# Kernel tuning notes

Hardware: AMD Instinct MI355X
Metric: run time of the kernel (lower is better)

## Reference

```python
import jax, jax.numpy as jnp
import numpy as np

R, E, NU, NI = 5, 50000, 20000, 20000
NF, DN, DR, DO = 4, 16, 64, 64   # num_factor, node/msg dim (64//NF), review dim (msg_units*NF), out_units
TAU = 0.5


def _l2norm(x):
    n = jnp.maximum(jnp.linalg.norm(x, axis=-1, keepdims=True), 1e-12)
    return x / n


def setup_inputs() -> dict:
    key = jax.random.key(0)
    ks = jax.random.split(key, 18)
    s = 0.1  # keep exp() arguments in a sane range / xavier-ish weight scale
    return {
        "user_h": jax.random.normal(ks[0], (NF, R, NU, DN), jnp.float32),
        "item_h": jax.random.normal(ks[1], (NF, R, NI, DN), jnp.float32),
        "user_hsum": jax.random.normal(ks[2], (R, NU, NF, DN), jnp.float32) * s,
        "item_hsum": jax.random.normal(ks[3], (R, NI, NF, DN), jnp.float32) * s,
        "review_feat": jax.random.normal(ks[4], (R, E, NF, DR), jnp.float32) * s,
        "prototypes": jax.random.normal(ks[5], (NF, DR), jnp.float32) * s,
        "eta": jax.random.normal(ks[6], (R, E), jnp.float32),
        "node_w_fwd": jax.random.normal(ks[7], (R, DN, DN), jnp.float32) * s,
        "review_w_fwd": jax.random.normal(ks[8], (R, DN, DR), jnp.float32) * s,
        "node_w_rev": jax.random.normal(ks[9], (R, DN, DN), jnp.float32) * s,
        "review_w_rev": jax.random.normal(ks[10], (R, DN, DR), jnp.float32) * s,
        "ufc_w": jax.random.normal(ks[11], (DO, DN), jnp.float32) * s,
        "ufc_b": jnp.zeros((DO,), jnp.float32),
        "ifc_w": jax.random.normal(ks[12], (DO, DN), jnp.float32) * s,
        "ifc_b": jnp.zeros((DO,), jnp.float32),
        "edge_src": jax.random.randint(ks[13], (R, E), 0, NU),
        "edge_dst": jax.random.randint(ks[14], (R, E), 0, NI),
        "k": 1,
    }


def reference(user_h, item_h, user_hsum, item_hsum, review_feat, prototypes,
              eta, node_w_fwd, review_w_fwd, node_w_rev, review_w_rev,
              ufc_w, ufc_b, ifc_w, ifc_b, edge_src, edge_dst, k):
    rI = jnp.arange(R)[:, None]                       # [R,1] rating index for gathers
    uh, ih = user_h[k], item_h[k]                     # [R,N,DN]
    # contrastive similarity on factor k (L2-normalized node feats)
    row_f = _l2norm(uh[rI, edge_src])                 # [R,E,DN]
    col_f = _l2norm(ih[rI, edge_dst])
    sim_k = jnp.sum(row_f * col_f, -1) / TAU          # [R,E]
    row_all = user_hsum[rI, edge_src]                 # [R,E,NF,DN]
    col_all = item_hsum[rI, edge_dst]
    sim_all = jnp.sum(row_all * col_all, -1) / TAU    # [R,E,NF]
    exp_sim = jnp.exp(sim_k) / jnp.sum(jnp.exp(sim_all), -1)
    # prototype (anchor) similarity of review features
    rf_k = review_feat[:, :, k, :]                    # [R,E,DR]
    anchor_k = jnp.einsum('red,d->re', rf_k, prototypes[k]) / TAU
    anchor_all = jnp.einsum('refd,fd->ref', review_feat, prototypes) / TAU
    exp_anchor = jnp.exp(anchor_k) / jnp.sum(jnp.exp(anchor_all), -1)
    g = jax.nn.sigmoid(eta)                           # eta[rating][:E]
    # identical for 'rating' and 'rev-rating' etypes (all dots commute under row/col swap)
    blended = g * exp_anchor + (1.0 - g) * exp_sim    # [R,E]
    flat = blended.reshape(-1)
    src_flat = edge_src.reshape(-1)
    dst_flat = edge_dst.reshape(-1)
    # fwd and rev etypes each contribute an identical scatter; (x + x) / 2 == x
    norm_user = jax.ops.segment_sum(flat, src_flat, num_segments=NU)
    norm_item = jax.ops.segment_sum(flat, dst_flat, num_segments=NI)
    n_ij = jnp.sqrt(norm_user[edge_src] * norm_item[edge_dst])  # [R,E]
    w = blended / n_ij                                # edge weight, same for both directions
    int_dist = w.reshape(R * E, 1)                    # concat of rev-etype weights in rating order
    # GCMCGraphConv per etype: (node_w(h_src)[row] + review_w(rf)) * w, scatter-sum to dst
    hu = jnp.einsum('rnd,rod->rno', uh, node_w_fwd)   # Linear: x @ W.T, per rating
    hi = jnp.einsum('rnd,rod->rno', ih, node_w_rev)
    rfw = jnp.einsum('red,rod->reo', rf_k, review_w_fwd)
    rfr = jnp.einsum('red,rod->reo', rf_k, review_w_rev)
    m_fwd = (hu[rI, edge_src] + rfw) * w[..., None]   # [R,E,DN] user->item messages
    m_rev = (hi[rI, edge_dst] + rfr) * w[..., None]   # item->user messages
    item_msg = jax.ops.segment_sum(m_fwd.reshape(-1, DN), dst_flat, num_segments=NI)
    user_msg = jax.ops.segment_sum(m_rev.reshape(-1, DN), src_flat, num_segments=NU)
    ufeat = jax.nn.leaky_relu(user_msg, 0.1) @ ufc_w.T + ufc_b
    ifeat = jax.nn.leaky_relu(item_msg, 0.1) @ ifc_w.T + ifc_b
    return ufeat, ifeat, int_dist
```

## Files before the change

### kernel.cpp

```cpp
#include <hip/hip_runtime.h>
#include <math.h>

constexpr int R  = 5;
constexpr int E  = 50000;
constexpr int NU = 20000;
constexpr int NI = 20000;
constexpr int NF = 4;
constexpr int DN = 16;
constexpr int DR = 64;
constexpr int DO = 64;
constexpr float TAU = 0.5f;
constexpr float INV_TAU = 2.0f;

__global__ __launch_bounds__(256) void pass1_kernel(
    const float* __restrict__ user_h,
    const float* __restrict__ item_h,
    const float* __restrict__ user_hsum,
    const float* __restrict__ item_hsum,
    const float* __restrict__ review_feat,
    const float* __restrict__ prototypes,
    const float* __restrict__ eta,
    const int*   __restrict__ edge_src,
    const int*   __restrict__ edge_dst,
    const int*   __restrict__ kptr,
    float* __restrict__ blended_out,
    float* __restrict__ norm_user,
    float* __restrict__ norm_item)
{
    const int lane = threadIdx.x & 63;
    const int w    = threadIdx.x >> 6;
    const int r    = blockIdx.y;
    const int base = (blockIdx.x * 4 + w) * 4;
    const int k    = *kptr;

    const int e  = lane >> 4;
    const int le = lane & 15;
    const int f  = le >> 2;
    const int j  = le & 3;

    const int ee = base + e;
    const long long re = (long long)r * E + ee;

    const int src = edge_src[re];
    const int dst = edge_dst[re];

    float na = 0.f, nb = 0.f, ab = 0.f;
    if (f == 0) {
        const float4 ua = *(const float4*)(user_h + (((long long)k * R + r) * NU + src) * DN + j * 4);
        const float4 ia = *(const float4*)(item_h + (((long long)k * R + r) * NI + dst) * DN + j * 4);
        na = ua.x*ua.x + ua.y*ua.y + ua.z*ua.z + ua.w*ua.w;
        nb = ia.x*ia.x + ia.y*ia.y + ia.z*ia.z + ia.w*ia.w;
        ab = ua.x*ia.x + ua.y*ia.y + ua.z*ia.z + ua.w*ia.w;
    }
    na += __shfl_xor(na, 1, 64); na += __shfl_xor(na, 2, 64);
    nb += __shfl_xor(nb, 1, 64); nb += __shfl_xor(nb, 2, 64);
    ab += __shfl_xor(ab, 1, 64); ab += __shfl_xor(ab, 2, 64);

    const float4 rs = *(const float4*)(user_hsum + ((long long)r * NU + src) * (NF * DN) + le * 4);
    const float4 cs = *(const float4*)(item_hsum + ((long long)r * NI + dst) * (NF * DN) + le * 4);
    float p = rs.x*cs.x + rs.y*cs.y + rs.z*cs.z + rs.w*cs.w;
    p += __shfl_xor(p, 1, 64); p += __shfl_xor(p, 2, 64);
    float denom_sim = __expf(p * INV_TAU);
    denom_sim += __shfl_xor(denom_sim, 4, 64);
    denom_sim += __shfl_xor(denom_sim, 8, 64);

    const float4* rf4 = (const float4*)review_feat + re * (NF * DR / 4);
    const float4* pr4 = (const float4*)prototypes;
    float q = 0.f;
#pragma unroll
    for (int c = 0; c < 4; ++c) {
        const float4 a = rf4[f * 16 + c * 4 + j];
        const float4 b = pr4[f * 16 + c * 4 + j];
        q += a.x*b.x + a.y*b.y + a.z*b.z + a.w*b.w;
    }
    q += __shfl_xor(q, 1, 64); q += __shfl_xor(q, 2, 64);
    float ea = __expf(q * INV_TAU);
    float denom_anc = ea;
    denom_anc += __shfl_xor(denom_anc, 4, 64);
    denom_anc += __shfl_xor(denom_anc, 8, 64);
    const float ea_k = __shfl(ea, (lane & 48) | (k << 2), 64);

    if (le == 0) {
        const float sim_k = ab / (fmaxf(sqrtf(na), 1e-12f) * fmaxf(sqrtf(nb), 1e-12f)) * INV_TAU;
        const float exp_anchor = ea_k / denom_anc;
        const float exp_sim    = __expf(sim_k) / denom_sim;
        const float g = 1.0f / (1.0f + __expf(-eta[re]));
        const float blended = g * exp_anchor + (1.0f - g) * exp_sim;
        blended_out[re] = blended;
        atomicAdd(&norm_user[src], blended);
        atomicAdd(&norm_item[dst], blended);
    }
}

__global__ __launch_bounds__(256) void nodexf_kernel(
    const float* __restrict__ user_h,
    const float* __restrict__ item_h,
    const float* __restrict__ node_w_fwd,
    const float* __restrict__ node_w_rev,
    const int*   __restrict__ kptr,
    float* __restrict__ hu_t,
    float* __restrict__ hi_t)
{
    const int r    = blockIdx.y;
    const int side = blockIdx.z;
    const int n0   = blockIdx.x * 64;
    const int k    = *kptr;
    const int N    = side ? NI : NU;
    const float* h    = side ? item_h : user_h;
    const float* wsrc = side ? node_w_rev : node_w_fwd;
    float* out        = side ? hi_t : hu_t;

    __shared__ __align__(16) float lds_h[64 * 16];
    __shared__ float lds_w[16 * 17];

    const int t = threadIdx.x;
    {
        const int o = t >> 4, d = t & 15;
        lds_w[o * 17 + d] = wsrc[((long long)r * DN + o) * DN + d];
    }
    {
        const int row = t >> 2, c = t & 3;
        if (n0 + row < N) {
            const float4 v = *(const float4*)(h + (((long long)k * R + r) * N + n0 + row) * DN + c * 4);
            *(float4*)&lds_h[t * 4] = v;
        }
    }
    __syncthreads();

    const int o = t & 15;
#pragma unroll
    for (int p = 0; p < 4; ++p) {
        const int nl = p * 16 + (t >> 4);
        const int n = n0 + nl;
        if (n < N) {
            float acc = 0.f;
#pragma unroll
            for (int d = 0; d < DN; ++d)
                acc += lds_h[nl * 16 + d] * lds_w[o * 17 + d];
            out[((long long)r * N + n) * DN + o] = acc;
        }
    }
}

__global__ __launch_bounds__(256) void pass2b_kernel(
    const float* __restrict__ hu_t,
    const float* __restrict__ hi_t,
    const float* __restrict__ review_feat,
    const float* __restrict__ review_w_fwd,
    const float* __restrict__ review_w_rev,
    const int*   __restrict__ edge_src,
    const int*   __restrict__ edge_dst,
    const int*   __restrict__ kptr,
    const float* __restrict__ blended,
    const float* __restrict__ norm_user,
    const float* __restrict__ norm_item,
    float* __restrict__ user_msg,
    float* __restrict__ item_msg,
    float* __restrict__ int_dist)
{
    constexpr int EPB = 64;
    constexpr int RSTRIDE = 68;
    constexpr int TSTRIDE = 17;
    const int r    = blockIdx.y;
    const int e0   = blockIdx.x * EPB;
    const int k    = *kptr;
    const int t    = threadIdx.x;
    const int lane = t & 63;
    const int w    = t >> 6;

    __shared__ __align__(16) float wf[DN * DR];
    __shared__ __align__(16) float wr[DN * DR];
    __shared__ __align__(16) float rf[EPB * RSTRIDE];
    __shared__ float wgt_s[EPB];
    __shared__ int   src_s[EPB];
    __shared__ int   dst_s[EPB];

    {
        const int i = t * 4;
        *(float4*)&wf[i] = *(const float4*)(review_w_fwd + (long long)r * (DN * DR) + i);
        *(float4*)&wr[i] = *(const float4*)(review_w_rev + (long long)r * (DN * DR) + i);
    }
    {
        const int row = t >> 2;
        const int c0  = (t & 3) * 16;
        const int ee  = e0 + row;
        if (ee < E) {
            const float4* s = (const float4*)(review_feat +
                (((long long)r * E + ee) * NF + k) * DR + c0);
            float4* d = (float4*)&rf[row * RSTRIDE + c0];
            d[0] = s[0]; d[1] = s[1]; d[2] = s[2]; d[3] = s[3];
        }
    }
    if (t < EPB) {
        const int ee = e0 + t;
        if (ee < E) {
            const long long re = (long long)r * E + ee;
            const int s  = edge_src[re];
            const int d2 = edge_dst[re];
            src_s[t] = s; dst_s[t] = d2;
            const float wgt = blended[re] * rsqrtf(norm_user[s] * norm_item[d2]);
            wgt_s[t] = wgt;
            int_dist[re] = wgt;
        }
    }
    __syncthreads();

    const int ee = e0 + lane;
    const int ob = w * 4;
    float accf[4] = {0.f, 0.f, 0.f, 0.f};
    float accr[4] = {0.f, 0.f, 0.f, 0.f};

    const float* rfrow = &rf[lane * RSTRIDE];
#pragma unroll 4
    for (int c = 0; c < 16; ++c) {
        const float4 a = *(const float4*)&rfrow[c * 4];
#pragma unroll
        for (int jj = 0; jj < 4; ++jj) {
            const float4 bf = *(const float4*)&wf[(ob + jj) * DR + c * 4];
            const float4 br = *(const float4*)&wr[(ob + jj) * DR + c * 4];
            accf[jj] += a.x*bf.x + a.y*bf.y + a.z*bf.z + a.w*bf.w;
            accr[jj] += a.x*br.x + a.y*br.y + a.z*br.z + a.w*br.w;
        }
    }

    float msgf[4] = {0.f, 0.f, 0.f, 0.f};
    float msgr[4] = {0.f, 0.f, 0.f, 0.f};
    if (ee < E) {
        const int src = src_s[lane];
        const int dst = dst_s[lane];
        const float wgt = wgt_s[lane];
        const float4 hu = *(const float4*)(hu_t + ((long long)r * NU + src) * DN + ob);
        const float4 hi = *(const float4*)(hi_t + ((long long)r * NI + dst) * DN + ob);
        msgf[0] = (accf[0] + hu.x) * wgt;  msgf[1] = (accf[1] + hu.y) * wgt;
        msgf[2] = (accf[2] + hu.z) * wgt;  msgf[3] = (accf[3] + hu.w) * wgt;
        msgr[0] = (accr[0] + hi.x) * wgt;  msgr[1] = (accr[1] + hi.y) * wgt;
        msgr[2] = (accr[2] + hi.z) * wgt;  msgr[3] = (accr[3] + hi.w) * wgt;
    }

    __syncthreads();
    float* af = rf;
    float* ar = rf + EPB * TSTRIDE;
#pragma unroll
    for (int jj = 0; jj < 4; ++jj) {
        af[lane * TSTRIDE + ob + jj] = msgf[jj];
        ar[lane * TSTRIDE + ob + jj] = msgr[jj];
    }
    __syncthreads();

    const int o  = t & 15;
    const int eb = t >> 4;
#pragma unroll
    for (int p = 0; p < 4; ++p) {
        const int el = eb + p * 16;
        if (e0 + el < E) {
            atomicAdd(&item_msg[(long long)dst_s[el] * DN + o], af[el * TSTRIDE + o]);
            atomicAdd(&user_msg[(long long)src_s[el] * DN + o], ar[el * TSTRIDE + o]);
        }
    }
}

__global__ __launch_bounds__(256) void pass3_kernel(
    const float* __restrict__ user_msg,
    const float* __restrict__ item_msg,
    const float* __restrict__ ufc_w,
    const float* __restrict__ ufc_b,
    const float* __restrict__ ifc_w,
    const float* __restrict__ ifc_b,
    float* __restrict__ ufeat,
    float* __restrict__ ifeat)
{
    const long long t = (long long)blockIdx.x * blockDim.x + threadIdx.x;
    const long long nu_total = (long long)NU * DO;
    const long long total = nu_total + (long long)NI * DO;
    if (t >= total) return;
    const bool is_item = (t >= nu_total);
    const long long tt = is_item ? (t - nu_total) : t;
    const int j = (int)(tt & 63);
    const long long n = tt >> 6;

    const float* msg  = (is_item ? item_msg : user_msg) + n * DN;
    const float* wrow = (is_item ? ifc_w : ufc_w) + (long long)j * DN;
    float acc = (is_item ? ifc_b : ufc_b)[j];
#pragma unroll
    for (int d = 0; d < DN; ++d) {
        float x = msg[d];
        x = (x > 0.f) ? x : 0.1f * x;
        acc += x * wrow[d];
    }
    (is_item ? ifeat : ufeat)[tt] = acc;
}

extern "C" void kernel_launch(void* const* d_in, const int* in_sizes, int n_in,
                              void* d_out, int out_size, void* d_ws, size_t ws_size,
                              hipStream_t stream) {
    const float* user_h       = (const float*)d_in[0];
    const float* item_h       = (const float*)d_in[1];
    const float* user_hsum    = (const float*)d_in[2];
    const float* item_hsum    = (const float*)d_in[3];
    const float* review_feat  = (const float*)d_in[4];
    const float* prototypes   = (const float*)d_in[5];
    const float* eta          = (const float*)d_in[6];
    const float* node_w_fwd   = (const float*)d_in[7];
    const float* review_w_fwd = (const float*)d_in[8];
    const float* node_w_rev   = (const float*)d_in[9];
    const float* review_w_rev = (const float*)d_in[10];
    const float* ufc_w        = (const float*)d_in[11];
    const float* ufc_b        = (const float*)d_in[12];
    const float* ifc_w        = (const float*)d_in[13];
    const float* ifc_b        = (const float*)d_in[14];
    const int*   edge_src     = (const int*)d_in[15];
    const int*   edge_dst     = (const int*)d_in[16];
    const int*   kptr         = (const int*)d_in[17];

    float* ws = (float*)d_ws;
    float* norm_user = ws;
    float* norm_item = norm_user + NU;
    float* user_msg  = norm_item + NI;
    float* item_msg  = user_msg + (long long)NU * DN;
    float* blended   = item_msg + (long long)NI * DN;
    float* hu_t      = blended + (long long)R * E;
    float* hi_t      = hu_t + (long long)R * NU * DN;

    const size_t zero_bytes = (size_t)(NU + NI + NU * DN + NI * DN) * sizeof(float);
    hipMemsetAsync(d_ws, 0, zero_bytes, stream);

    float* ufeat    = (float*)d_out;
    float* ifeat    = ufeat + (long long)NU * DO;
    float* int_dist = ifeat + (long long)NI * DO;

    {
        dim3 grid((NU + 63) / 64, R, 2);
        nodexf_kernel<<<grid, 256, 0, stream>>>(
            user_h, item_h, node_w_fwd, node_w_rev, kptr, hu_t, hi_t);
    }

    {
        dim3 grid(E / 16, R);
        pass1_kernel<<<grid, 256, 0, stream>>>(
            user_h, item_h, user_hsum, item_hsum, review_feat, prototypes,
            eta, edge_src, edge_dst, kptr, blended, norm_user, norm_item);
    }

    {
        dim3 grid((E + 63) / 64, R);
        pass2b_kernel<<<grid, 256, 0, stream>>>(
            hu_t, hi_t, review_feat, review_w_fwd, review_w_rev,
            edge_src, edge_dst, kptr, blended, norm_user, norm_item,
            user_msg, item_msg, int_dist);
    }

    {
        const long long nthreads = (long long)(NU + NI) * DO;
        const int blocks = (int)((nthreads + 255) / 256);
        pass3_kernel<<<blocks, 256, 0, stream>>>(
            user_msg, item_msg, ufc_w, ufc_b, ifc_w, ifc_b, ufeat, ifeat);
    }
}
```

Before: 494.5 us.

## Replace float atomic scatter with CSR bucketing and per-node gather reduction

Edge-to-node message scatter no longer uses per-element float atomics. Degrees are now counted in pass1, a single-block scan builds CSR offsets, and edge ids are bucketed with integer atomics. Per-edge messages are written densely, then a gather kernel sums each node's incoming messages. This removes float atomic contention, but it adds extra kernels, a large message buffer write and read (about 32 MB), scattered gathers, and a serial scan over 20000 nodes run on one block per side.

After: 550.0 us. 11.2% more time.

```diff
diff --git a/kernel.cpp b/kernel.cpp
--- a/kernel.cpp
+++ b/kernel.cpp
@@ -25,7 +25,9 @@
     const int*   __restrict__ kptr,
     float* __restrict__ blended_out,
     float* __restrict__ norm_user,
-    float* __restrict__ norm_item)
+    float* __restrict__ norm_item,
+    int*   __restrict__ deg_u,
+    int*   __restrict__ deg_i)
 {
     const int lane = threadIdx.x & 63;
     const int w    = threadIdx.x >> 6;
@@ -89,6 +91,8 @@
         blended_out[re] = blended;
         atomicAdd(&norm_user[src], blended);
         atomicAdd(&norm_item[dst], blended);
+        atomicAdd(&deg_u[src], 1);
+        atomicAdd(&deg_i[dst], 1);
     }
 }
 
@@ -142,7 +146,48 @@
     }
 }
 
-__global__ __launch_bounds__(256) void pass2b_kernel(
+__global__ __launch_bounds__(1024) void scan_kernel(
+    const int* __restrict__ deg_u, const int* __restrict__ deg_i,
+    int* __restrict__ off_u, int* __restrict__ off_i,
+    int* __restrict__ cur_u, int* __restrict__ cur_i)
+{
+    constexpr int N = NU;
+    constexpr int CHUNK = 20;
+    const int side = blockIdx.x;
+    const int* deg = side ? deg_i : deg_u;
+    int* off = side ? off_i : off_u;
+    int* cur = side ? cur_i : cur_u;
+
+    __shared__ int s[1024];
+    const int t  = threadIdx.x;
+    const int i0 = t * CHUNK;
+
+    int local[CHUNK];
+    int sum = 0;
+#pragma unroll
+    for (int i = 0; i < CHUNK; ++i) {
+        const int idx = i0 + i;
+        const int v = (idx < N) ? deg[idx] : 0;
+        local[i] = v; sum += v;
+    }
+    s[t] = sum;
+    __syncthreads();
+    for (int d = 1; d < 1024; d <<= 1) {
+        const int v = (t >= d) ? s[t - d] : 0;
+        __syncthreads();
+        s[t] += v;
+        __syncthreads();
+    }
+    int run = s[t] - sum;
+#pragma unroll
+    for (int i = 0; i < CHUNK; ++i) {
+        const int idx = i0 + i;
+        if (idx < N) { off[idx] = run; cur[idx] = run; run += local[i]; }
+    }
+    if (t == 1023) off[N] = s[1023];
+}
+
+__global__ __launch_bounds__(256) void pass2w_kernel(
     const float* __restrict__ hu_t,
     const float* __restrict__ hi_t,
     const float* __restrict__ review_feat,
@@ -154,8 +199,12 @@
     const float* __restrict__ blended,
     const float* __restrict__ norm_user,
     const float* __restrict__ norm_item,
-    float* __restrict__ user_msg,
-    float* __restrict__ item_msg,
+    int*   __restrict__ cur_u,
+    int*   __restrict__ cur_i,
+    int*   __restrict__ elist_u,
+    int*   __restrict__ elist_i,
+    float* __restrict__ msg_fwd,
+    float* __restrict__ msg_rev,
     float* __restrict__ int_dist)
 {
     constexpr int EPB = 64;
@@ -201,6 +250,10 @@
             const float wgt = blended[re] * rsqrtf(norm_user[s] * norm_item[d2]);
             wgt_s[t] = wgt;
             int_dist[re] = wgt;
+            const int slot_u = atomicAdd(&cur_u[s], 1);
+            elist_u[slot_u] = (int)re;
+            const int slot_i = atomicAdd(&cur_i[d2], 1);
+            elist_i[slot_i] = (int)re;
         }
     }
     __syncthreads();
@@ -252,11 +305,46 @@
 #pragma unroll
     for (int p = 0; p < 4; ++p) {
         const int el = eb + p * 16;
-        if (e0 + el < E) {
-            atomicAdd(&item_msg[(long long)dst_s[el] * DN + o], af[el * TSTRIDE + o]);
-            atomicAdd(&user_msg[(long long)src_s[el] * DN + o], ar[el * TSTRIDE + o]);
-        }
-    }
+        const int ee2 = e0 + el;
+        if (ee2 < E) {
+            const long long re2 = (long long)r * E + ee2;
+            msg_fwd[re2 * DN + o] = af[el * TSTRIDE + o];
+            msg_rev[re2 * DN + o] = ar[el * TSTRIDE + o];
+        }
+    }
+}
+
+__global__ __launch_bounds__(256) void gather_kernel(
+    const float* __restrict__ msg_rev,
+    const float* __restrict__ msg_fwd,
+    const int*   __restrict__ off_u, const int* __restrict__ off_i,
+    const int*   __restrict__ elist_u, const int* __restrict__ elist_i,
+    float* __restrict__ user_msg,
+    float* __restrict__ item_msg)
+{
+    const int side  = blockIdx.y;
+    const int t     = threadIdx.x;
+    const int le    = t & 15;
+    const int g     = t >> 4;
+    const int n     = blockIdx.x * 16 + g;
+    if (n >= NU) return;
+
+    const int*   off = side ? off_i : off_u;
+    const int*   el  = side ? elist_i : elist_u;
+    const float* msg = side ? msg_fwd : msg_rev;
+
+    const int j0 = off[n], j1 = off[n + 1];
+    float acc0 = 0.f, acc1 = 0.f;
+    int j = j0;
+    for (; j + 1 < j1; j += 2) {
+        const int ea = el[j];
+        const int eb = el[j + 1];
+        acc0 += msg[(long long)ea * DN + le];
+        acc1 += msg[(long long)eb * DN + le];
+    }
+    if (j < j1) acc0 += msg[(long long)el[j] * DN + le];
+
+    (side ? item_msg : user_msg)[(long long)n * DN + le] = acc0 + acc1;
 }
 
 __global__ __launch_bounds__(256) void pass3_kernel(
@@ -313,16 +401,26 @@
     const int*   kptr         = (const int*)d_in[17];
 
     float* ws = (float*)d_ws;
-    float* norm_user = ws;
-    float* norm_item = norm_user + NU;
-    float* user_msg  = norm_item + NI;
+    float* hu_t      = ws;
+    float* hi_t      = hu_t + (long long)R * NU * DN;
+    float* msg_fwd   = hi_t + (long long)R * NI * DN;
+    float* msg_rev   = msg_fwd + (long long)R * E * DN;
+    float* user_msg  = msg_rev + (long long)R * E * DN;
     float* item_msg  = user_msg + (long long)NU * DN;
     float* blended   = item_msg + (long long)NI * DN;
-    float* hu_t      = blended + (long long)R * E;
-    float* hi_t      = hu_t + (long long)R * NU * DN;
-
-    const size_t zero_bytes = (size_t)(NU + NI + NU * DN + NI * DN) * sizeof(float);
-    hipMemsetAsync(d_ws, 0, zero_bytes, stream);
+    float* norm_user = blended + (long long)R * E;
+    float* norm_item = norm_user + NU;
+    int*   deg_u     = (int*)(norm_item + NI);
+    int*   deg_i     = deg_u + NU;
+    int*   off_u     = deg_i + NI;
+    int*   off_i     = off_u + (NU + 1);
+    int*   cur_u     = off_i + (NI + 1);
+    int*   cur_i     = cur_u + NU;
+    int*   elist_u   = cur_i + NI;
+    int*   elist_i   = elist_u + (long long)R * E;
+
+    const size_t zero_bytes = (size_t)(NU + NI) * 2 * sizeof(float);
+    hipMemsetAsync(norm_user, 0, zero_bytes, stream);
 
     float* ufeat    = (float*)d_out;
     float* ifeat    = ufeat + (long long)NU * DO;
@@ -338,15 +436,28 @@
         dim3 grid(E / 16, R);
         pass1_kernel<<<grid, 256, 0, stream>>>(
             user_h, item_h, user_hsum, item_hsum, review_feat, prototypes,
-            eta, edge_src, edge_dst, kptr, blended, norm_user, norm_item);
+            eta, edge_src, edge_dst, kptr, blended, norm_user, norm_item,
+            deg_u, deg_i);
+    }
+
+    {
+        scan_kernel<<<dim3(2), 1024, 0, stream>>>(
+            deg_u, deg_i, off_u, off_i, cur_u, cur_i);
     }
 
     {
         dim3 grid((E + 63) / 64, R);
-        pass2b_kernel<<<grid, 256, 0, stream>>>(
+        pass2w_kernel<<<grid, 256, 0, stream>>>(
             hu_t, hi_t, review_feat, review_w_fwd, review_w_rev,
             edge_src, edge_dst, kptr, blended, norm_user, norm_item,
-            user_msg, item_msg, int_dist);
+            cur_u, cur_i, elist_u, elist_i, msg_fwd, msg_rev, int_dist);
+    }
+
+    {
+        dim3 grid((NU + 15) / 16, 2);
+        gather_kernel<<<grid, 256, 0, stream>>>(
+            msg_rev, msg_fwd, off_u, off_i, elist_u, elist_i,
+            user_msg, item_msg);
     }
 
     {
```

## Fuse all stages into one persistent cooperative kernel with grid syncs

Applied to the files above, without the earlier changes.

Merges the memset, node transform, edge weight pass, message pass and output projection into one cooperative kernel. Blocks loop over work units and are separated by grid-wide syncs. This removes four kernel launches and the separate memset, replacing launch gaps with grid barriers. In exchange, occupancy is capped by the persistent grid size (assumed 256 CUs, at most 8 blocks each), grid.sync has its own cost, and the larger shared buffer may reduce occupancy.

Result: slower. 740.6 us (+49.8%).

```diff
diff --git a/kernel.cpp b/kernel.cpp
--- a/kernel.cpp
+++ b/kernel.cpp
@@ -1,5 +1,8 @@
 #include <hip/hip_runtime.h>
+#include <hip/hip_cooperative_groups.h>
 #include <math.h>
+
+namespace cg = cooperative_groups;
 
 constexpr int R  = 5;
 constexpr int E  = 50000;
@@ -12,7 +15,16 @@
 constexpr float TAU = 0.5f;
 constexpr float INV_TAU = 2.0f;
 
-__global__ __launch_bounds__(256) void pass1_kernel(
+constexpr int NXF_TILES  = (NU + 63) / 64;
+constexpr int NXF_UNITS  = NXF_TILES * R * 2;
+constexpr int P1_TILES   = E / 16;
+constexpr int P1_UNITS   = P1_TILES * R;
+constexpr int P2_TILES   = (E + 63) / 64;
+constexpr int P2_UNITS   = P2_TILES * R;
+constexpr long long ZTOT4 = (long long)(NU + NI) * (DN + 1) / 4;
+constexpr long long P3_TOT = (long long)(NU + NI) * DO;
+
+__global__ __launch_bounds__(256) void fused_kernel(
     const float* __restrict__ user_h,
     const float* __restrict__ item_h,
     const float* __restrict__ user_hsum,
@@ -20,274 +32,286 @@
     const float* __restrict__ review_feat,
     const float* __restrict__ prototypes,
     const float* __restrict__ eta,
-    const int*   __restrict__ edge_src,
-    const int*   __restrict__ edge_dst,
-    const int*   __restrict__ kptr,
-    float* __restrict__ blended_out,
-    float* __restrict__ norm_user,
-    float* __restrict__ norm_item)
-{
-    const int lane = threadIdx.x & 63;
-    const int w    = threadIdx.x >> 6;
-    const int r    = blockIdx.y;
-    const int base = (blockIdx.x * 4 + w) * 4;
-    const int k    = *kptr;
-
-    const int e  = lane >> 4;
-    const int le = lane & 15;
-    const int f  = le >> 2;
-    const int j  = le & 3;
-
-    const int ee = base + e;
-    const long long re = (long long)r * E + ee;
-
-    const int src = edge_src[re];
-    const int dst = edge_dst[re];
-
-    float na = 0.f, nb = 0.f, ab = 0.f;
-    if (f == 0) {
-        const float4 ua = *(const float4*)(user_h + (((long long)k * R + r) * NU + src) * DN + j * 4);
-        const float4 ia = *(const float4*)(item_h + (((long long)k * R + r) * NI + dst) * DN + j * 4);
-        na = ua.x*ua.x + ua.y*ua.y + ua.z*ua.z + ua.w*ua.w;
-        nb = ia.x*ia.x + ia.y*ia.y + ia.z*ia.z + ia.w*ia.w;
-        ab = ua.x*ia.x + ua.y*ia.y + ua.z*ia.z + ua.w*ia.w;
-    }
-    na += __shfl_xor(na, 1, 64); na += __shfl_xor(na, 2, 64);
-    nb += __shfl_xor(nb, 1, 64); nb += __shfl_xor(nb, 2, 64);
-    ab += __shfl_xor(ab, 1, 64); ab += __shfl_xor(ab, 2, 64);
-
-    const float4 rs = *(const float4*)(user_hsum + ((long long)r * NU + src) * (NF * DN) + le * 4);
-    const float4 cs = *(const float4*)(item_hsum + ((long long)r * NI + dst) * (NF * DN) + le * 4);
-    float p = rs.x*cs.x + rs.y*cs.y + rs.z*cs.z + rs.w*cs.w;
-    p += __shfl_xor(p, 1, 64); p += __shfl_xor(p, 2, 64);
-    float denom_sim = __expf(p * INV_TAU);
-    denom_sim += __shfl_xor(denom_sim, 4, 64);
-    denom_sim += __shfl_xor(denom_sim, 8, 64);
-
-    const float4* rf4 = (const float4*)review_feat + re * (NF * DR / 4);
-    const float4* pr4 = (const float4*)prototypes;
-    float q = 0.f;
-#pragma unroll
-    for (int c = 0; c < 4; ++c) {
-        const float4 a = rf4[f * 16 + c * 4 + j];
-        const float4 b = pr4[f * 16 + c * 4 + j];
-        q += a.x*b.x + a.y*b.y + a.z*b.z + a.w*b.w;
-    }
-    q += __shfl_xor(q, 1, 64); q += __shfl_xor(q, 2, 64);
-    float ea = __expf(q * INV_TAU);
-    float denom_anc = ea;
-    denom_anc += __shfl_xor(denom_anc, 4, 64);
-    denom_anc += __shfl_xor(denom_anc, 8, 64);
-    const float ea_k = __shfl(ea, (lane & 48) | (k << 2), 64);
-
-    if (le == 0) {
-        const float sim_k = ab / (fmaxf(sqrtf(na), 1e-12f) * fmaxf(sqrtf(nb), 1e-12f)) * INV_TAU;
-        const float exp_anchor = ea_k / denom_anc;
-        const float exp_sim    = __expf(sim_k) / denom_sim;
-        const float g = 1.0f / (1.0f + __expf(-eta[re]));
-        const float blended = g * exp_anchor + (1.0f - g) * exp_sim;
-        blended_out[re] = blended;
-        atomicAdd(&norm_user[src], blended);
-        atomicAdd(&norm_item[dst], blended);
-    }
-}
-
-__global__ __launch_bounds__(256) void nodexf_kernel(
-    const float* __restrict__ user_h,
-    const float* __restrict__ item_h,
     const float* __restrict__ node_w_fwd,
+    const float* __restrict__ review_w_fwd,
     const float* __restrict__ node_w_rev,
-    const int*   __restrict__ kptr,
-    float* __restrict__ hu_t,
-    float* __restrict__ hi_t)
-{
-    const int r    = blockIdx.y;
-    const int side = blockIdx.z;
-    const int n0   = blockIdx.x * 64;
-    const int k    = *kptr;
-    const int N    = side ? NI : NU;
-    const float* h    = side ? item_h : user_h;
-    const float* wsrc = side ? node_w_rev : node_w_fwd;
-    float* out        = side ? hi_t : hu_t;
-
-    __shared__ __align__(16) float lds_h[64 * 16];
-    __shared__ float lds_w[16 * 17];
-
-    const int t = threadIdx.x;
-    {
-        const int o = t >> 4, d = t & 15;
-        lds_w[o * 17 + d] = wsrc[((long long)r * DN + o) * DN + d];
-    }
-    {
-        const int row = t >> 2, c = t & 3;
-        if (n0 + row < N) {
-            const float4 v = *(const float4*)(h + (((long long)k * R + r) * N + n0 + row) * DN + c * 4);
-            *(float4*)&lds_h[t * 4] = v;
-        }
-    }
-    __syncthreads();
-
-    const int o = t & 15;
-#pragma unroll
-    for (int p = 0; p < 4; ++p) {
-        const int nl = p * 16 + (t >> 4);
-        const int n = n0 + nl;
-        if (n < N) {
-            float acc = 0.f;
-#pragma unroll
-            for (int d = 0; d < DN; ++d)
-                acc += lds_h[nl * 16 + d] * lds_w[o * 17 + d];
-            out[((long long)r * N + n) * DN + o] = acc;
-        }
-    }
-}
-
-__global__ __launch_bounds__(256) void pass2b_kernel(
-    const float* __restrict__ hu_t,
-    const float* __restrict__ hi_t,
-    const float* __restrict__ review_feat,
-    const float* __restrict__ review_w_fwd,
     const float* __restrict__ review_w_rev,
-    const int*   __restrict__ edge_src,
-    const int*   __restrict__ edge_dst,
-    const int*   __restrict__ kptr,
-    const float* __restrict__ blended,
-    const float* __restrict__ norm_user,
-    const float* __restrict__ norm_item,
-    float* __restrict__ user_msg,
-    float* __restrict__ item_msg,
-    float* __restrict__ int_dist)
-{
-    constexpr int EPB = 64;
-    constexpr int RSTRIDE = 68;
-    constexpr int TSTRIDE = 17;
-    const int r    = blockIdx.y;
-    const int e0   = blockIdx.x * EPB;
-    const int k    = *kptr;
-    const int t    = threadIdx.x;
-    const int lane = t & 63;
-    const int w    = t >> 6;
-
-    __shared__ __align__(16) float wf[DN * DR];
-    __shared__ __align__(16) float wr[DN * DR];
-    __shared__ __align__(16) float rf[EPB * RSTRIDE];
-    __shared__ float wgt_s[EPB];
-    __shared__ int   src_s[EPB];
-    __shared__ int   dst_s[EPB];
-
-    {
-        const int i = t * 4;
-        *(float4*)&wf[i] = *(const float4*)(review_w_fwd + (long long)r * (DN * DR) + i);
-        *(float4*)&wr[i] = *(const float4*)(review_w_rev + (long long)r * (DN * DR) + i);
-    }
-    {
-        const int row = t >> 2;
-        const int c0  = (t & 3) * 16;
-        const int ee  = e0 + row;
-        if (ee < E) {
-            const float4* s = (const float4*)(review_feat +
-                (((long long)r * E + ee) * NF + k) * DR + c0);
-            float4* d = (float4*)&rf[row * RSTRIDE + c0];
-            d[0] = s[0]; d[1] = s[1]; d[2] = s[2]; d[3] = s[3];
-        }
-    }
-    if (t < EPB) {
-        const int ee = e0 + t;
-        if (ee < E) {
-            const long long re = (long long)r * E + ee;
-            const int s  = edge_src[re];
-            const int d2 = edge_dst[re];
-            src_s[t] = s; dst_s[t] = d2;
-            const float wgt = blended[re] * rsqrtf(norm_user[s] * norm_item[d2]);
-            wgt_s[t] = wgt;
-            int_dist[re] = wgt;
-        }
-    }
-    __syncthreads();
-
-    const int ee = e0 + lane;
-    const int ob = w * 4;
-    float accf[4] = {0.f, 0.f, 0.f, 0.f};
-    float accr[4] = {0.f, 0.f, 0.f, 0.f};
-
-    const float* rfrow = &rf[lane * RSTRIDE];
-#pragma unroll 4
-    for (int c = 0; c < 16; ++c) {
-        const float4 a = *(const float4*)&rfrow[c * 4];
-#pragma unroll
-        for (int jj = 0; jj < 4; ++jj) {
-            const float4 bf = *(const float4*)&wf[(ob + jj) * DR + c * 4];
-            const float4 br = *(const float4*)&wr[(ob + jj) * DR + c * 4];
-            accf[jj] += a.x*bf.x + a.y*bf.y + a.z*bf.z + a.w*bf.w;
-            accr[jj] += a.x*br.x + a.y*br.y + a.z*br.z + a.w*br.w;
-        }
-    }
-
-    float msgf[4] = {0.f, 0.f, 0.f, 0.f};
-    float msgr[4] = {0.f, 0.f, 0.f, 0.f};
-    if (ee < E) {
-        const int src = src_s[lane];
-        const int dst = dst_s[lane];
-        const float wgt = wgt_s[lane];
-        const float4 hu = *(const float4*)(hu_t + ((long long)r * NU + src) * DN + ob);
-        const float4 hi = *(const float4*)(hi_t + ((long long)r * NI + dst) * DN + ob);
-        msgf[0] = (accf[0] + hu.x) * wgt;  msgf[1] = (accf[1] + hu.y) * wgt;
-        msgf[2] = (accf[2] + hu.z) * wgt;  msgf[3] = (accf[3] + hu.w) * wgt;
-        msgr[0] = (accr[0] + hi.x) * wgt;  msgr[1] = (accr[1] + hi.y) * wgt;
-        msgr[2] = (accr[2] + hi.z) * wgt;  msgr[3] = (accr[3] + hi.w) * wgt;
-    }
-
-    __syncthreads();
-    float* af = rf;
-    float* ar = rf + EPB * TSTRIDE;
-#pragma unroll
-    for (int jj = 0; jj < 4; ++jj) {
-        af[lane * TSTRIDE + ob + jj] = msgf[jj];
-        ar[lane * TSTRIDE + ob + jj] = msgr[jj];
-    }
-    __syncthreads();
-
-    const int o  = t & 15;
-    const int eb = t >> 4;
-#pragma unroll
-    for (int p = 0; p < 4; ++p) {
-        const int el = eb + p * 16;
-        if (e0 + el < E) {
-            atomicAdd(&item_msg[(long long)dst_s[el] * DN + o], af[el * TSTRIDE + o]);
-            atomicAdd(&user_msg[(long long)src_s[el] * DN + o], ar[el * TSTRIDE + o]);
-        }
-    }
-}
-
-__global__ __launch_bounds__(256) void pass3_kernel(
-    const float* __restrict__ user_msg,
-    const float* __restrict__ item_msg,
     const float* __restrict__ ufc_w,
     const float* __restrict__ ufc_b,
     const float* __restrict__ ifc_w,
     const float* __restrict__ ifc_b,
+    const int*   __restrict__ edge_src,
+    const int*   __restrict__ edge_dst,
+    const int*   __restrict__ kptr,
+    float* __restrict__ norm_user,
+    float* __restrict__ norm_item,
+    float* __restrict__ user_msg,
+    float* __restrict__ item_msg,
+    float* __restrict__ blended,
+    float* __restrict__ hu_t,
+    float* __restrict__ hi_t,
+    float* __restrict__ int_dist,
     float* __restrict__ ufeat,
     float* __restrict__ ifeat)
 {
-    const long long t = (long long)blockIdx.x * blockDim.x + threadIdx.x;
-    const long long nu_total = (long long)NU * DO;
-    const long long total = nu_total + (long long)NI * DO;
-    if (t >= total) return;
-    const bool is_item = (t >= nu_total);
-    const long long tt = is_item ? (t - nu_total) : t;
-    const int j = (int)(tt & 63);
-    const long long n = tt >> 6;
-
-    const float* msg  = (is_item ? item_msg : user_msg) + n * DN;
-    const float* wrow = (is_item ? ifc_w : ufc_w) + (long long)j * DN;
-    float acc = (is_item ? ifc_b : ufc_b)[j];
-#pragma unroll
-    for (int d = 0; d < DN; ++d) {
-        float x = msg[d];
-        x = (x > 0.f) ? x : 0.1f * x;
-        acc += x * wrow[d];
-    }
-    (is_item ? ifeat : ufeat)[tt] = acc;
+    cg::grid_group grid = cg::this_grid();
+
+    const int t    = threadIdx.x;
+    const int lane = t & 63;
+    const int w    = t >> 6;
+    const int k    = *kptr;
+
+    __shared__ __align__(16) float smem[6592];
+
+    {
+        float4 z = make_float4(0.f, 0.f, 0.f, 0.f);
+        for (long long i = (long long)blockIdx.x * 256 + t; i < ZTOT4;
+             i += (long long)gridDim.x * 256)
+            ((float4*)norm_user)[i] = z;
+    }
+
+    {
+        float* lds_h = smem;
+        float* lds_w = smem + 1024;
+        for (int unit = blockIdx.x; unit < NXF_UNITS; unit += gridDim.x) {
+            const int n0   = (unit % NXF_TILES) * 64;
+            const int rs   = unit / NXF_TILES;
+            const int r    = rs % R;
+            const int side = rs / R;
+            const int N    = side ? NI : NU;
+            const float* h    = side ? item_h : user_h;
+            const float* wsrc = side ? node_w_rev : node_w_fwd;
+            float* out        = side ? hi_t : hu_t;
+
+            {
+                const int o = t >> 4, d = t & 15;
+                lds_w[o * 17 + d] = wsrc[((long long)r * DN + o) * DN + d];
+            }
+            {
+                const int row = t >> 2, c = t & 3;
+                if (n0 + row < N) {
+                    const float4 v = *(const float4*)(h +
+                        (((long long)k * R + r) * N + n0 + row) * DN + c * 4);
+                    *(float4*)&lds_h[t * 4] = v;
+                }
+            }
+            __syncthreads();
+
+            const int o = t & 15;
+#pragma unroll
+            for (int p = 0; p < 4; ++p) {
+                const int nl = p * 16 + (t >> 4);
+                const int n = n0 + nl;
+                if (n < N) {
+                    float acc = 0.f;
+#pragma unroll
+                    for (int d = 0; d < DN; ++d)
+                        acc += lds_h[nl * 16 + d] * lds_w[o * 17 + d];
+                    out[((long long)r * N + n) * DN + o] = acc;
+                }
+            }
+            __syncthreads();
+        }
+    }
+
+    grid.sync();
+
+    {
+        const int e  = lane >> 4;
+        const int le = lane & 15;
+        const int f  = le >> 2;
+        const int j  = le & 3;
+
+        for (int unit = blockIdx.x; unit < P1_UNITS; unit += gridDim.x) {
+            const int r    = unit / P1_TILES;
+            const int tile = unit % P1_TILES;
+            const int base = (tile * 4 + w) * 4;
+            const int ee   = base + e;
+            const long long re = (long long)r * E + ee;
+
+            const int src = edge_src[re];
+            const int dst = edge_dst[re];
+
+            float na = 0.f, nb = 0.f, ab = 0.f;
+            if (f == 0) {
+                const float4 ua = *(const float4*)(user_h +
+                    (((long long)k * R + r) * NU + src) * DN + j * 4);
+                const float4 ia = *(const float4*)(item_h +
+                    (((long long)k * R + r) * NI + dst) * DN + j * 4);
+                na = ua.x*ua.x + ua.y*ua.y + ua.z*ua.z + ua.w*ua.w;
+                nb = ia.x*ia.x + ia.y*ia.y + ia.z*ia.z + ia.w*ia.w;
+                ab = ua.x*ia.x + ua.y*ia.y + ua.z*ia.z + ua.w*ia.w;
+            }
+            na += __shfl_xor(na, 1, 64); na += __shfl_xor(na, 2, 64);
+            nb += __shfl_xor(nb, 1, 64); nb += __shfl_xor(nb, 2, 64);
+            ab += __shfl_xor(ab, 1, 64); ab += __shfl_xor(ab, 2, 64);
+
+            const float4 rs4 = *(const float4*)(user_hsum +
+                ((long long)r * NU + src) * (NF * DN) + le * 4);
+            const float4 cs4 = *(const float4*)(item_hsum +
+                ((long long)r * NI + dst) * (NF * DN) + le * 4);
+            float p = rs4.x*cs4.x + rs4.y*cs4.y + rs4.z*cs4.z + rs4.w*cs4.w;
+            p += __shfl_xor(p, 1, 64); p += __shfl_xor(p, 2, 64);
+            float denom_sim = __expf(p * INV_TAU);
+            denom_sim += __shfl_xor(denom_sim, 4, 64);
+            denom_sim += __shfl_xor(denom_sim, 8, 64);
+
+            const float4* rf4 = (const float4*)review_feat + re * (NF * DR / 4);
+            const float4* pr4 = (const float4*)prototypes;
+            float q = 0.f;
+#pragma unroll
+            for (int c = 0; c < 4; ++c) {
+                const float4 a = rf4[f * 16 + c * 4 + j];
+                const float4 b = pr4[f * 16 + c * 4 + j];
+                q += a.x*b.x + a.y*b.y + a.z*b.z + a.w*b.w;
+            }
+            q += __shfl_xor(q, 1, 64); q += __shfl_xor(q, 2, 64);
+            float ea = __expf(q * INV_TAU);
+            float denom_anc = ea;
+            denom_anc += __shfl_xor(denom_anc, 4, 64);
+            denom_anc += __shfl_xor(denom_anc, 8, 64);
+            const float ea_k = __shfl(ea, (lane & 48) | (k << 2), 64);
+
+            if (le == 0) {
+                const float sim_k = ab /
+                    (fmaxf(sqrtf(na), 1e-12f) * fmaxf(sqrtf(nb), 1e-12f)) * INV_TAU;
+                const float exp_anchor = ea_k / denom_anc;
+                const float exp_sim    = __expf(sim_k) / denom_sim;
+                const float g = 1.0f / (1.0f + __expf(-eta[re]));
+                const float bl = g * exp_anchor + (1.0f - g) * exp_sim;
+                blended[re] = bl;
+                atomicAdd(&norm_user[src], bl);
+                atomicAdd(&norm_item[dst], bl);
+            }
+        }
+    }
+
+    grid.sync();
+
+    {
+        constexpr int EPB = 64;
+        constexpr int RSTRIDE = 68;
+        constexpr int TSTRIDE = 17;
+        float* wf    = smem;
+        float* wr    = smem + 1024;
+        float* rf    = smem + 2048;
+        float* wgt_s = smem + 6400;
+        int*   src_s = (int*)(smem + 6464);
+        int*   dst_s = (int*)(smem + 6528);
+
+        for (int unit = blockIdx.x; unit < P2_UNITS; unit += gridDim.x) {
+            const int r  = unit / P2_TILES;
+            const int e0 = (unit % P2_TILES) * EPB;
+
+            {
+                const int i = t * 4;
+                *(float4*)&wf[i] = *(const float4*)(review_w_fwd + (long long)r * (DN * DR) + i);
+                *(float4*)&wr[i] = *(const float4*)(review_w_rev + (long long)r * (DN * DR) + i);
+            }
+            {
+                const int row = t >> 2;
+                const int c0  = (t & 3) * 16;
+                const int ee  = e0 + row;
+                if (ee < E) {
+                    const float4* s = (const float4*)(review_feat +
+                        (((long long)r * E + ee) * NF + k) * DR + c0);
+                    float4* d = (float4*)&rf[row * RSTRIDE + c0];
+                    d[0] = s[0]; d[1] = s[1]; d[2] = s[2]; d[3] = s[3];
+                }
+            }
+            if (t < EPB) {
+                const int ee = e0 + t;
+                if (ee < E) {
+                    const long long re = (long long)r * E + ee;
+                    const int s  = edge_src[re];
+                    const int d2 = edge_dst[re];
+                    src_s[t] = s; dst_s[t] = d2;
+                    const float wgt = blended[re] * rsqrtf(norm_user[s] * norm_item[d2]);
+                    wgt_s[t] = wgt;
+                    int_dist[re] = wgt;
+                }
+            }
+            __syncthreads();
+
+            const int ee = e0 + lane;
+            const int ob = w * 4;
+            float accf[4] = {0.f, 0.f, 0.f, 0.f};
+            float accr[4] = {0.f, 0.f, 0.f, 0.f};
+
+            const float* rfrow = &rf[lane * RSTRIDE];
+#pragma unroll 4
+            for (int c = 0; c < 16; ++c) {
+                const float4 a = *(const float4*)&rfrow[c * 4];
+#pragma unroll
+                for (int jj = 0; jj < 4; ++jj) {
+                    const float4 bf = *(const float4*)&wf[(ob + jj) * DR + c * 4];
+                    const float4 br = *(const float4*)&wr[(ob + jj) * DR + c * 4];
+                    accf[jj] += a.x*bf.x + a.y*bf.y + a.z*bf.z + a.w*bf.w;
+                    accr[jj] += a.x*br.x + a.y*br.y + a.z*br.z + a.w*br.w;
+                }
+            }
+
+            float msgf[4] = {0.f, 0.f, 0.f, 0.f};
+            float msgr[4] = {0.f, 0.f, 0.f, 0.f};
+            if (ee < E) {
+                const int src = src_s[lane];
+                const int dst = dst_s[lane];
+                const float wgt = wgt_s[lane];
+                const float4 hu = *(const float4*)(hu_t + ((long long)r * NU + src) * DN + ob);
+                const float4 hi = *(const float4*)(hi_t + ((long long)r * NI + dst) * DN + ob);
+                msgf[0] = (accf[0] + hu.x) * wgt;  msgf[1] = (accf[1] + hu.y) * wgt;
+                msgf[2] = (accf[2] + hu.z) * wgt;  msgf[3] = (accf[3] + hu.w) * wgt;
+                msgr[0] = (accr[0] + hi.x) * wgt;  msgr[1] = (accr[1] + hi.y) * wgt;
+                msgr[2] = (accr[2] + hi.z) * wgt;  msgr[3] = (accr[3] + hi.w) * wgt;
+            }
+
+            __syncthreads();
+            float* af = rf;
+            float* ar = rf + EPB * TSTRIDE;
+#pragma unroll
+            for (int jj = 0; jj < 4; ++jj) {
+                af[lane * TSTRIDE + ob + jj] = msgf[jj];
+                ar[lane * TSTRIDE + ob + jj] = msgr[jj];
+            }
+            __syncthreads();
+
+            const int o  = t & 15;
+            const int eb = t >> 4;
+#pragma unroll
+            for (int p = 0; p < 4; ++p) {
+                const int el = eb + p * 16;
+                if (e0 + el < E) {
+                    atomicAdd(&item_msg[(long long)dst_s[el] * DN + o], af[el * TSTRIDE + o]);
+                    atomicAdd(&user_msg[(long long)src_s[el] * DN + o], ar[el * TSTRIDE + o]);
+                }
+            }
+            __syncthreads();
+        }
+    }
+
+    grid.sync();
+
+    {
+        const long long nu_total = (long long)NU * DO;
+        for (long long u = (long long)blockIdx.x * 256 + t; u < P3_TOT;
+             u += (long long)gridDim.x * 256) {
+            const bool is_item = (u >= nu_total);
+            const long long tt = is_item ? (u - nu_total) : u;
+            const int j = (int)(tt & 63);
+            const long long n = tt >> 6;
+
+            const float* msg  = (is_item ? item_msg : user_msg) + n * DN;
+            const float* wrow = (is_item ? ifc_w : ufc_w) + (long long)j * DN;
+            float acc = (is_item ? ifc_b : ufc_b)[j];
+#pragma unroll
+            for (int d = 0; d < DN; ++d) {
+                float x = msg[d];
+                x = (x > 0.f) ? x : 0.1f * x;
+                acc += x * wrow[d];
+            }
+            (is_item ? ifeat : ufeat)[tt] = acc;
+        }
+    }
 }
 
 extern "C" void kernel_launch(void* const* d_in, const int* in_sizes, int n_in,
@@ -321,38 +345,26 @@
     float* hu_t      = blended + (long long)R * E;
     float* hi_t      = hu_t + (long long)R * NU * DN;
 
-    const size_t zero_bytes = (size_t)(NU + NI + NU * DN + NI * DN) * sizeof(float);
-    hipMemsetAsync(d_ws, 0, zero_bytes, stream);
-
     float* ufeat    = (float*)d_out;
     float* ifeat    = ufeat + (long long)NU * DO;
     float* int_dist = ifeat + (long long)NI * DO;
 
-    {
-        dim3 grid((NU + 63) / 64, R, 2);
-        nodexf_kernel<<<grid, 256, 0, stream>>>(
-            user_h, item_h, node_w_fwd, node_w_rev, kptr, hu_t, hi_t);
-    }
-
-    {
-        dim3 grid(E / 16, R);
-        pass1_kernel<<<grid, 256, 0, stream>>>(
-            user_h, item_h, user_hsum, item_hsum, review_feat, prototypes,
-            eta, edge_src, edge_dst, kptr, blended, norm_user, norm_item);
-    }
-
-    {
-        dim3 grid((E + 63) / 64, R);
-        pass2b_kernel<<<grid, 256, 0, stream>>>(
-            hu_t, hi_t, review_feat, review_w_fwd, review_w_rev,
-            edge_src, edge_dst, kptr, blended, norm_user, norm_item,
-            user_msg, item_msg, int_dist);
-    }
-
-    {
-        const long long nthreads = (long long)(NU + NI) * DO;
-        const int blocks = (int)((nthreads + 255) / 256);
-        pass3_kernel<<<blocks, 256, 0, stream>>>(
-            user_msg, item_msg, ufc_w, ufc_b, ifc_w, ifc_b, ufeat, ifeat);
-    }
+    int nbpc = 0;
+    if (hipOccupancyMaxActiveBlocksPerMultiprocessor(&nbpc, fused_kernel, 256, 0)
+            != hipSuccess || nbpc < 1)
+        nbpc = 1;
+    if (nbpc > 8) nbpc = 8;
+    const int nblk = nbpc * 256;
+
+    void* args[] = {
+        (void*)&user_h, (void*)&item_h, (void*)&user_hsum, (void*)&item_hsum,
+        (void*)&review_feat, (void*)&prototypes, (void*)&eta,
+        (void*)&node_w_fwd, (void*)&review_w_fwd, (void*)&node_w_rev,
+        (void*)&review_w_rev, (void*)&ufc_w, (void*)&ufc_b, (void*)&ifc_w,
+        (void*)&ifc_b, (void*)&edge_src, (void*)&edge_dst, (void*)&kptr,
+        (void*)&norm_user, (void*)&norm_item, (void*)&user_msg, (void*)&item_msg,
+        (void*)&blended, (void*)&hu_t, (void*)&hi_t, (void*)&int_dist,
+        (void*)&ufeat, (void*)&ifeat
+    };
+    hipLaunchCooperativeKernel(fused_kernel, dim3(nblk), dim3(256), args, 0, stream);
 }
```
